# Performance work log

Measured on AMD Instinct MI355X. Metric: run time of the kernel, lower is better.

The kernel has to match this reference:

```python
import jax, jax.numpy as jnp
import numpy as np

HIDDEN = 128
N_HID = 7            # hidden_layers - 1 internal GELU blocks
N_TERMS = 2          # number of separable terms per side
N_IN = 1             # vars per term
B = 16384
STEP_SIZE = 0.1
NUM_STEPS = 1

# Forest-Ruth 4th-order symplectic coefficients
_K = 2.0 ** (1.0 / 3.0)
_C = (1.0 / (2.0 * (2.0 - _K)), (1.0 - _K) / (2.0 * (2.0 - _K)),
      (1.0 - _K) / (2.0 * (2.0 - _K)), 1.0 / (2.0 * (2.0 - _K)))
_D = (1.0 / (2.0 - _K), -_K / (2.0 - _K), 1.0 / (2.0 - _K), 0.0)


def _mlp(W0, b0, Wh, bh, Wo, bo, x):
    # x: [B, n_in] -> [B, 1]; torch GELU default is exact (erf)
    h = jax.nn.gelu(x @ W0 + b0, approximate=False)
    for i in range(N_HID):
        h = jax.nn.gelu(h @ Wh[i] + bh[i], approximate=False)
    return h @ Wo + bo


def _side_scalar(W0, b0, Wh, bh, Wo, bo, idx, x):
    # gather per-term feature subsets, run all term-MLPs batched via vmap,
    # sum over terms and batch (GradientWrapper takes grad of the summed scalar)
    xs = jnp.moveaxis(x[:, idx], 1, 0)            # [n_terms, B, n_in]
    outs = jax.vmap(_mlp)(W0, b0, Wh, bh, Wo, bo, xs)  # [n_terms, B, 1]
    return outs.sum()


def setup_inputs() -> dict:
    key = jax.random.key(0)
    ks = jax.random.split(key, 3)
    s = 0.05

    def pset(k):
        kk = jax.random.split(k, 6)
        return (
            jax.random.normal(kk[0], (N_TERMS, N_IN, HIDDEN), jnp.float32) * s,
            jax.random.normal(kk[1], (N_TERMS, HIDDEN), jnp.float32) * s,
            jax.random.normal(kk[2], (N_TERMS, N_HID, HIDDEN, HIDDEN), jnp.float32) * s,
            jax.random.normal(kk[3], (N_TERMS, N_HID, HIDDEN), jnp.float32) * s,
            jax.random.normal(kk[4], (N_TERMS, HIDDEN, 1), jnp.float32) * s,
            jax.random.normal(kk[5], (N_TERMS, 1), jnp.float32) * s,
        )

    lW0, lb0, lWh, lbh, lWo, lbo = pset(ks[0])
    rW0, rb0, rWh, rbh, rWo, rbo = pset(ks[1])
    X = jax.random.normal(ks[2], (B, 4), jnp.float32)
    left_idx = jnp.arange(N_TERMS, dtype=jnp.int32).reshape(N_TERMS, N_IN)
    right_idx = jnp.arange(N_TERMS, dtype=jnp.int32).reshape(N_TERMS, N_IN)
    return dict(X=X, lW0=lW0, lb0=lb0, lWh=lWh, lbh=lbh, lWo=lWo, lbo=lbo,
                rW0=rW0, rb0=rb0, rWh=rWh, rbh=rbh, rWo=rWo, rbo=rbo,
                left_idx=left_idx, right_idx=right_idx)


def reference(X, lW0, lb0, lWh, lbh, lWo, lbo,
              rW0, rb0, rWh, rbh, rWo, rbo, left_idx, right_idx):
    # H(q, p) = V(q) + T(p); left side = V(q), right side = T(p)
    dVdq = jax.grad(lambda q: _side_scalar(lW0, lb0, lWh, lbh, lWo, lbo, left_idx, q))
    dTdp = jax.grad(lambda p: _side_scalar(rW0, rb0, rWh, rbh, rWo, rbo, right_idx, p))
    dt = jnp.float32(STEP_SIZE)
    nq = X.shape[1] // 2
    q = X[:, :nq]
    p = X[:, nq:]
    for _ in range(NUM_STEPS):
        for c, d in zip(_C, _D):
            q = q + jnp.float32(c) * dt * dTdp(p)   # dq/dt =  dH/dp
            p = p - jnp.float32(d) * dt * dVdq(q)   # dp/dt = -dH/dq
    return jnp.concatenate((q, p), axis=1)
```

## Files before the change

kernel.cpp:

```cpp
#include <hip/hip_runtime.h>

#define NLAYER 7
#define IMGB 16384
#define WSCALE 16.0f

typedef __attribute__((ext_vector_type(2))) float float2v;
typedef __attribute__((ext_vector_type(4))) float float4v;
typedef __attribute__((ext_vector_type(4))) unsigned int uint4v;
typedef __attribute__((ext_vector_type(4))) int int4v;
typedef __attribute__((ext_vector_type(8))) int int8v;
typedef unsigned long long u64;

__device__ __forceinline__ float2v pk_fma(float2v a, float2v b, float2v c){
  return __builtin_elementwise_fma(a, b, c);
}
__device__ __forceinline__ float2v lo2(float4v v){ return (float2v){v[0], v[1]}; }
__device__ __forceinline__ float2v hi2(float4v v){ return (float2v){v[2], v[3]}; }

__device__ __forceinline__ unsigned pk4fp8(float v0, float v1, float v2, float v3){
  int w = __builtin_amdgcn_cvt_pk_fp8_f32(v0, v1, 0, false);
  w = __builtin_amdgcn_cvt_pk_fp8_f32(v2, v3, w, true);
  return (unsigned)w;
}
template<bool HI>
__device__ __forceinline__ float2v up2(unsigned w){
  return __builtin_amdgcn_cvt_pk_f32_fp8((int)w, HI);
}
__device__ __forceinline__ float4v mfma128(int8v a, int8v b){
  return __builtin_amdgcn_mfma_scale_f32_16x16x128_f8f6f4(
      a, b, (float4v){0.f,0.f,0.f,0.f}, 0, 0, 0, 0x7F7F7F7F, 0, 0x7F7F7F7F);
}
__device__ __forceinline__ void act2(float2v z, float2v& P16, float2v& gp16){
  const float2v c1v  = {6.3830764862829235f, 6.3830764862829235f};
  const float2v c3v  = {-1.0638460810704874f, -1.0638460810704874f};
  const float2v c33v = {-3.1915382432114624f, -3.1915382432114624f};
  const float2v v8   = {8.f, 8.f};
  float2v z2 = z * z;
  float2v u  = pk_fma(z2, c3v, c1v);
  P16 = pk_fma(z, u, v8);
  float2v Pd = pk_fma(z2, c33v, c1v);
  gp16 = pk_fma(z, Pd, P16);
}

__device__ __forceinline__ void gl2lds16(const unsigned char* g, unsigned char* l){
  __builtin_amdgcn_global_load_lds((const __attribute__((address_space(1))) unsigned int*)g,
                                   (__attribute__((address_space(3))) unsigned int*)l,
                                   16, 0, 0);
}

__device__ __forceinline__ int8v ld_op16(const unsigned char* lp, const unsigned char* hp){
  int4v lo = *(const int4v*)lp;
  int4v hi = *(const int4v*)hp;
  return __builtin_shufflevector(lo, hi, 0, 1, 2, 3, 4, 5, 6, 7);
}

__global__ __launch_bounds__(256)
void prep_weights(const float* __restrict__ lWh,
                  const float* __restrict__ rWh,
                  unsigned char* __restrict__ wbf)
{
  __shared__ __align__(16) unsigned char T[IMGB];
  const int b = blockIdx.x;
  const int net = b / NLAYER, L = b % NLAYER;
  const int side = net >> 1, term = net & 1;
  const float* src = (side ? rWh : lWh) + (size_t)((term*NLAYER + L)*128)*128;
  const int t = threadIdx.x;
  {
    const int k = t >> 1, n0 = (t & 1)*64;
    const float* row = src + k*128 + n0;
    #pragma unroll
    for (int c4 = 0; c4 < 4; ++c4){
      float4v f0 = *(const float4v*)(row + c4*16);
      float4v f1 = *(const float4v*)(row + c4*16 + 4);
      float4v f2 = *(const float4v*)(row + c4*16 + 8);
      float4v f3 = *(const float4v*)(row + c4*16 + 12);
      uint4v wv = { pk4fp8(f0[0]*WSCALE, f0[1]*WSCALE, f0[2]*WSCALE, f0[3]*WSCALE),
                    pk4fp8(f1[0]*WSCALE, f1[1]*WSCALE, f1[2]*WSCALE, f1[3]*WSCALE),
                    pk4fp8(f2[0]*WSCALE, f2[1]*WSCALE, f2[2]*WSCALE, f2[3]*WSCALE),
                    pk4fp8(f3[0]*WSCALE, f3[1]*WSCALE, f3[2]*WSCALE, f3[3]*WSCALE) };
      *(uint4v*)&T[k*128 + n0 + c4*16] = wv;
    }
  }
  __syncthreads();
  {
    const int n = t >> 1, c0 = (t & 1)*8;
    const int sw7 = n & 7;
    unsigned char* dst = wbf + ((size_t)b << 14) + n*128;
    #pragma unroll
    for (int c = 0; c < 8; ++c){
      const int c64 = c0 + c;
      const int kc = c64*8;
      u64 v = 0;
      #pragma unroll
      for (int j = 0; j < 8; ++j)
        v |= (u64)T[(kc + j)*128 + n] << (8*j);
      *(u64*)(dst + (((c64 >> 1) ^ sw7)*16) + (c64 & 1)*8) = v;
    }
  }
}

__global__ __launch_bounds__(256)
__attribute__((amdgpu_waves_per_eu(4, 4)))
void sympl_main(const float* __restrict__ X,
                const float* __restrict__ lW0, const float* __restrict__ lb0,
                const float* __restrict__ lbh, const float* __restrict__ lWo,
                const float* __restrict__ rW0, const float* __restrict__ rb0,
                const float* __restrict__ rbh, const float* __restrict__ rWo,
                const int* __restrict__ lidx, const int* __restrict__ ridx,
                const unsigned char* __restrict__ wbf,
                float* __restrict__ out)
{
  __shared__ __align__(16) unsigned char sW[2][IMGB];
  __shared__ __align__(16) unsigned char sH[8192];

  const int tid  = threadIdx.x;
  const int lane = tid & 63;
  const int w    = tid >> 6;
  const int m0   = lane & 15;
  const int q    = lane >> 4;
  const int g    = w & 1;
  const int ih   = w >> 1;
  const int col  = blockIdx.y;
  const int e0   = blockIdx.x * 32;
  const int r    = tid >> 3;
  const int sg   = tid & 7;
  const int r7   = r & 7;
  const int m06  = m0 & 6;
  const int m07  = m0 & 7;

  const int lt = (lidx[0] == col) ? 0 : 1;
  const int rt = (ridx[0] == col) ? 0 : 1;

  float qv = X[(e0 + r)*4 + col];
  float pv = X[(e0 + r)*4 + 2 + col];

  const float dt = 0.1f;
  const float C0 = 0.6756035959798289f, C1 = -0.17560359597982883f;
  const float D0 = 1.3512071919596578f, D1 = -1.7024143839193153f;
  const float is = 1.0f / 262144.0f;
  const float coefs[7] = { C0*dt*is, -D0*dt*is, C1*dt*is, -D1*dt*is,
                           C1*dt*is, -D0*dt*is, C0*dt*is };

  const float2v inv256v = {1.f/256.f, 1.f/256.f};
  const float2v inv64v  = {1.f/64.f, 1.f/64.f};

  const int lo16 = (m0 & 1) * 16;
  const int opo  = ((2*q) ^ m06) * 16;
  const unsigned char* pB0lo = sH + (g*16 + m0)*128 + opo + lo16;
  const unsigned char* pB0hi = sH + (g*16 + m0)*128 + opo + 16 - lo16;
  const unsigned char* pA0lo = sW[0] + (ih*64 + m0)*128 + opo + lo16;
  const unsigned char* pA0hi = sW[0] + (ih*64 + m0)*128 + opo + 16 - lo16;
  unsigned char* pHe = sH + (g*16 + m0)*128;
  unsigned char* pL0 = sH + r*128 + ((sg ^ r7)*16);
  const unsigned char* pRd = sH + 4096 + r*128 + ((sg ^ r7)*16);
  const int q4 = q * 4;
  const int eo0 = ((ih*4 + 0) ^ m07)*16 + q4;
  const int eo1 = ((ih*4 + 1) ^ m07)*16 + q4;
  const int eo2 = ((ih*4 + 2) ^ m07)*16 + q4;
  const int eo3 = ((ih*4 + 3) ^ m07)*16 + q4;

  {
    const unsigned char* src = wbf + (size_t)(2 + rt)*NLAYER*IMGB;
    #pragma unroll
    for (int it = 0; it < 4; ++it){
      int o = (it*256 + tid) * 16;
      gl2lds16(src + o, sW[0] + o);
    }
  }
  __syncthreads();

  int cur = 0;

  for (int ev = 0; ev < 7; ++ev){
    const bool isT = !(ev & 1);
    const int  term = isT ? rt : lt;
    const float* W0p = (isT ? rW0 : lW0) + term*128;
    const float* b0p = (isT ? rb0 : lb0) + term*128;
    const float* bhp = (isT ? rbh : lbh) + term*NLAYER*128;
    const float* Wop = (isT ? rWo : lWo) + term*128;
    const unsigned char* wimg = wbf + (size_t)(((isT ? 2 : 0) + term)*NLAYER)*IMGB;
    const int tnx = (ev & 1) ? rt : lt;
    const unsigned char* wimg_nx = wbf + (size_t)((((ev & 1) ? 2 : 0) + tnx)*NLAYER)*IMGB;

    {
      const float x = isT ? pv : qv;
      const float2v xv = {x, x};
      unsigned hw[4], dw[4];
      #pragma unroll
      for (int c = 0; c < 2; ++c){
        int n0 = sg*16 + c*8;
        float4v wa = *(const float4v*)(W0p + n0);
        float4v wb = *(const float4v*)(W0p + n0 + 4);
        float4v ba = *(const float4v*)(b0p + n0);
        float4v bb2 = *(const float4v*)(b0p + n0 + 4);
        float2v zp[4] = { pk_fma(xv, lo2(wa), lo2(ba)), pk_fma(xv, hi2(wa), hi2(ba)),
                          pk_fma(xv, lo2(wb), lo2(bb2)), pk_fma(xv, hi2(wb), hi2(bb2)) };
        float2v wp[4] = { lo2(wa), hi2(wa), lo2(wb), hi2(wb) };
        float Sh[8], Sd[8];
        #pragma unroll
        for (int pp = 0; pp < 4; ++pp){
          float2v P16, gp16; act2(zp[pp], P16, gp16);
          float2v h = zp[pp] * P16;
          float2v d = gp16 * wp[pp];
          Sh[pp*2] = h[0]; Sh[pp*2+1] = h[1];
          Sd[pp*2] = d[0]; Sd[pp*2+1] = d[1];
        }
        hw[c*2]   = pk4fp8(Sh[0],Sh[1],Sh[2],Sh[3]);
        hw[c*2+1] = pk4fp8(Sh[4],Sh[5],Sh[6],Sh[7]);
        dw[c*2]   = pk4fp8(Sd[0],Sd[1],Sd[2],Sd[3]);
        dw[c*2+1] = pk4fp8(Sd[4],Sd[5],Sd[6],Sd[7]);
      }
      *(uint4v*)(pL0)        = (uint4v){hw[0], hw[1], hw[2], hw[3]};
      *(uint4v*)(pL0 + 4096) = (uint4v){dw[0], dw[1], dw[2], dw[3]};
    }
    __syncthreads();

    for (int L = 0; L < NLAYER; ++L){
      const float* bias = bhp + L*128 + ih*64 + q4;
      float4v bv0 = *(const float4v*)(bias);
      float4v bv1 = *(const float4v*)(bias + 16);
      float4v bv2 = *(const float4v*)(bias + 32);
      float4v bv3 = *(const float4v*)(bias + 48);

      if (!(ev == 6 && L == 6)){
        const unsigned char* nsrc = (L < 6) ? (wimg + (size_t)(L+1)*IMGB) : wimg_nx;
        unsigned char* dW = sW[cur^1];
        #pragma unroll
        for (int it = 0; it < 4; ++it){
          int o = (it*256 + tid) * 16;
          gl2lds16(nsrc + o, dW + o);
        }
      }

      const int bufo = cur ? IMGB : 0;
      const unsigned char* pAcLo = pA0lo + bufo;
      const unsigned char* pAcHi = pA0hi + bufo;
      int8v b0 = ld_op16(pB0lo, pB0hi);
      int8v b1 = ld_op16(pB0lo + 4096, pB0hi + 4096);
      float4v acc[4][2];
      #pragma unroll
      for (int i = 0; i < 4; ++i){
        int8v a = ld_op16(pAcLo + i*2048, pAcHi + i*2048);
        acc[i][0] = mfma128(a, b0);
        acc[i][1] = mfma128(a, b1);
      }

      asm volatile("s_waitcnt lgkmcnt(0)" ::: "memory");
      __builtin_amdgcn_s_barrier();
      asm volatile("" ::: "memory");

      const bool last = (L == NLAYER-1);
      #define EPI(i, bvv, eo) { \
        float2v za = pk_fma(lo2(acc[i][0]), inv256v, lo2(bvv)); \
        float2v zb = pk_fma(hi2(acc[i][0]), inv256v, hi2(bvv)); \
        float2v ta = lo2(acc[i][1]) * inv64v; \
        float2v tb = hi2(acc[i][1]) * inv64v; \
        float2v Pa, ga, Pb, gb; \
        act2(za, Pa, ga); \
        act2(zb, Pb, gb); \
        float2v ha = za * Pa, hb = zb * Pb; \
        float2v da = ga * ta, db = gb * tb; \
        if (!last) *(unsigned*)(pHe + eo) = pk4fp8(ha[0], ha[1], hb[0], hb[1]); \
        *(unsigned*)(pHe + 4096 + eo) = pk4fp8(da[0], da[1], db[0], db[1]); \
      }
      EPI(0, bv0, eo0)
      EPI(1, bv1, eo1)
      EPI(2, bv2, eo2)
      EPI(3, bv3, eo3)
      #undef EPI

      __syncthreads();
      cur ^= 1;
    }

    {
      uint4v dvv = *(const uint4v*)(pRd);
      float2v sv = {0.f, 0.f};
      float4v woa = *(const float4v*)(Wop + sg*16);
      float4v wob = *(const float4v*)(Wop + sg*16 + 4);
      float4v woc = *(const float4v*)(Wop + sg*16 + 8);
      float4v wod = *(const float4v*)(Wop + sg*16 + 12);
      sv = pk_fma(up2<false>(dvv[0]), lo2(woa), sv);
      sv = pk_fma(up2<true>(dvv[0]),  hi2(woa), sv);
      sv = pk_fma(up2<false>(dvv[1]), lo2(wob), sv);
      sv = pk_fma(up2<true>(dvv[1]),  hi2(wob), sv);
      sv = pk_fma(up2<false>(dvv[2]), lo2(woc), sv);
      sv = pk_fma(up2<true>(dvv[2]),  hi2(woc), sv);
      sv = pk_fma(up2<false>(dvv[3]), lo2(wod), sv);
      sv = pk_fma(up2<true>(dvv[3]),  hi2(wod), sv);
      float s = sv[0] + sv[1];
      s += __shfl_xor(s, 1);
      s += __shfl_xor(s, 2);
      s += __shfl_xor(s, 4);
      if (isT) qv += coefs[ev] * s;
      else     pv += coefs[ev] * s;
    }
    __syncthreads();
  }

  if (sg == 0){
    out[(e0 + r)*4 + col]     = qv;
    out[(e0 + r)*4 + 2 + col] = pv;
  }
}

extern "C" void kernel_launch(void* const* d_in, const int* in_sizes, int n_in,
                              void* d_out, int out_size, void* d_ws, size_t ws_size,
                              hipStream_t stream)
{
  const float* X   = (const float*)d_in[0];
  const float* lW0 = (const float*)d_in[1];
  const float* lb0 = (const float*)d_in[2];
  const float* lWh = (const float*)d_in[3];
  const float* lbh = (const float*)d_in[4];
  const float* lWo = (const float*)d_in[5];
  const float* rW0 = (const float*)d_in[7];
  const float* rb0 = (const float*)d_in[8];
  const float* rWh = (const float*)d_in[9];
  const float* rbh = (const float*)d_in[10];
  const float* rWo = (const float*)d_in[11];
  const int*   li  = (const int*)d_in[13];
  const int*   ri  = (const int*)d_in[14];
  unsigned char* wbf = (unsigned char*)d_ws;
  float* out = (float*)d_out;
  const int B = in_sizes[0] / 4;

  hipLaunchKernelGGL(prep_weights, dim3(4*NLAYER), dim3(256), 0, stream,
                     lWh, rWh, wbf);
  hipLaunchKernelGGL(sympl_main, dim3(B/32, 2), dim3(256), 0, stream,
                     X, lW0, lb0, lbh, lWo, rW0, rb0, rbh, rWo, li, ri, wbf, out);
}
```

Baseline: 192.2 us.

## Load weight operands directly into registers and double-buffer activations in LDS

The prep kernel now writes weights in a per-lane MFMA operand order, so each lane fetches its A fragments straight from global memory into registers. This replaces the global-to-LDS weight staging and its double buffer. The hidden-activation LDS buffer is double-buffered by layer parity, which drops one barrier per layer and the barrier after each evaluation. LDS use shrinks, which may help occupancy, but the next layer's weights now come from global/L2 into VGPRs and their latency may be exposed before the next layer's MFMAs.

```diff
diff --git a/kernel.cpp b/kernel.cpp
--- a/kernel.cpp
+++ b/kernel.cpp
@@ -40,12 +40,6 @@
   P16 = pk_fma(z, u, v8);
   float2v Pd = pk_fma(z2, c33v, c1v);
   gp16 = pk_fma(z, Pd, P16);
-}
-
-__device__ __forceinline__ void gl2lds16(const unsigned char* g, unsigned char* l){
-  __builtin_amdgcn_global_load_lds((const __attribute__((address_space(1))) unsigned int*)g,
-                                   (__attribute__((address_space(3))) unsigned int*)l,
-                                   16, 0, 0);
 }
 
 __device__ __forceinline__ int8v ld_op16(const unsigned char* lp, const unsigned char* hp){
@@ -84,8 +78,8 @@
   __syncthreads();
   {
     const int n = t >> 1, c0 = (t & 1)*8;
-    const int sw7 = n & 7;
-    unsigned char* dst = wbf + ((size_t)b << 14) + n*128;
+    const int ihn = n >> 6, in_ = (n >> 4) & 3, m0n = n & 15;
+    unsigned char* dst = wbf + ((size_t)b << 14);
     #pragma unroll
     for (int c = 0; c < 8; ++c){
       const int c64 = c0 + c;
@@ -94,7 +88,8 @@
       #pragma unroll
       for (int j = 0; j < 8; ++j)
         v |= (u64)T[(kc + j)*128 + n] << (8*j);
-      *(u64*)(dst + (((c64 >> 1) ^ sw7)*16) + (c64 & 1)*8) = v;
+      const int off = ((ihn*4 + (c64 >> 2))*16 + m0n)*128 + in_*32 + (kc & 31);
+      *(u64*)(dst + off) = v;
     }
   }
 }
@@ -110,8 +105,7 @@
                 const unsigned char* __restrict__ wbf,
                 float* __restrict__ out)
 {
-  __shared__ __align__(16) unsigned char sW[2][IMGB];
-  __shared__ __align__(16) unsigned char sH[8192];
+  __shared__ __align__(16) unsigned char sH[2*8192];
 
   const int tid  = threadIdx.x;
   const int lane = tid & 63;
@@ -148,28 +142,23 @@
   const int opo  = ((2*q) ^ m06) * 16;
   const unsigned char* pB0lo = sH + (g*16 + m0)*128 + opo + lo16;
   const unsigned char* pB0hi = sH + (g*16 + m0)*128 + opo + 16 - lo16;
-  const unsigned char* pA0lo = sW[0] + (ih*64 + m0)*128 + opo + lo16;
-  const unsigned char* pA0hi = sW[0] + (ih*64 + m0)*128 + opo + 16 - lo16;
   unsigned char* pHe = sH + (g*16 + m0)*128;
   unsigned char* pL0 = sH + r*128 + ((sg ^ r7)*16);
-  const unsigned char* pRd = sH + 4096 + r*128 + ((sg ^ r7)*16);
+  const unsigned char* pRd = sH + 8192 + 4096 + r*128 + ((sg ^ r7)*16);
   const int q4 = q * 4;
-  const int eo0 = ((ih*4 + 0) ^ m07)*16 + q4;
-  const int eo1 = ((ih*4 + 1) ^ m07)*16 + q4;
-  const int eo2 = ((ih*4 + 2) ^ m07)*16 + q4;
-  const int eo3 = ((ih*4 + 3) ^ m07)*16 + q4;
-
+  unsigned char* pE0 = pHe + ((ih*4 + 0) ^ m07)*16 + q4;
+  unsigned char* pE1 = pHe + ((ih*4 + 1) ^ m07)*16 + q4;
+  unsigned char* pE2 = pHe + ((ih*4 + 2) ^ m07)*16 + q4;
+  unsigned char* pE3 = pHe + ((ih*4 + 3) ^ m07)*16 + q4;
+
+  const int laneAoff = ((ih*4 + q)*16 + m0)*128;
+
+  int4v aC[8];
   {
-    const unsigned char* src = wbf + (size_t)(2 + rt)*NLAYER*IMGB;
+    const unsigned char* asrc = wbf + (size_t)(2 + rt)*NLAYER*IMGB + laneAoff;
     #pragma unroll
-    for (int it = 0; it < 4; ++it){
-      int o = (it*256 + tid) * 16;
-      gl2lds16(src + o, sW[0] + o);
-    }
-  }
-  __syncthreads();
-
-  int cur = 0;
+    for (int i = 0; i < 8; ++i) aC[i] = *(const int4v*)(asrc + i*16);
+  }
 
   for (int ev = 0; ev < 7; ++ev){
     const bool isT = !(ev & 1);
@@ -213,44 +202,39 @@
       *(uint4v*)(pL0)        = (uint4v){hw[0], hw[1], hw[2], hw[3]};
       *(uint4v*)(pL0 + 4096) = (uint4v){dw[0], dw[1], dw[2], dw[3]};
     }
-    __syncthreads();
-
+    asm volatile("s_waitcnt lgkmcnt(0)" ::: "memory");
+    __builtin_amdgcn_s_barrier();
+    asm volatile("" ::: "memory");
+
+    #pragma unroll
     for (int L = 0; L < NLAYER; ++L){
+      const int rdo = (L & 1) * 8192;
+      const int wro = rdo ^ 8192;
+
       const float* bias = bhp + L*128 + ih*64 + q4;
       float4v bv0 = *(const float4v*)(bias);
       float4v bv1 = *(const float4v*)(bias + 16);
       float4v bv2 = *(const float4v*)(bias + 32);
       float4v bv3 = *(const float4v*)(bias + 48);
 
-      if (!(ev == 6 && L == 6)){
-        const unsigned char* nsrc = (L < 6) ? (wimg + (size_t)(L+1)*IMGB) : wimg_nx;
-        unsigned char* dW = sW[cur^1];
-        #pragma unroll
-        for (int it = 0; it < 4; ++it){
-          int o = (it*256 + tid) * 16;
-          gl2lds16(nsrc + o, dW + o);
-        }
-      }
-
-      const int bufo = cur ? IMGB : 0;
-      const unsigned char* pAcLo = pA0lo + bufo;
-      const unsigned char* pAcHi = pA0hi + bufo;
-      int8v b0 = ld_op16(pB0lo, pB0hi);
-      int8v b1 = ld_op16(pB0lo + 4096, pB0hi + 4096);
+      int8v b0 = ld_op16(pB0lo + rdo, pB0hi + rdo);
+      int8v b1 = ld_op16(pB0lo + rdo + 4096, pB0hi + rdo + 4096);
       float4v acc[4][2];
       #pragma unroll
       for (int i = 0; i < 4; ++i){
-        int8v a = ld_op16(pAcLo + i*2048, pAcHi + i*2048);
+        int8v a = __builtin_shufflevector(aC[2*i], aC[2*i+1], 0, 1, 2, 3, 4, 5, 6, 7);
         acc[i][0] = mfma128(a, b0);
         acc[i][1] = mfma128(a, b1);
       }
 
-      asm volatile("s_waitcnt lgkmcnt(0)" ::: "memory");
-      __builtin_amdgcn_s_barrier();
-      asm volatile("" ::: "memory");
+      if (!(ev == 6 && L == 6)){
+        const unsigned char* nsrc = ((L < 6) ? (wimg + (size_t)(L+1)*IMGB) : wimg_nx) + laneAoff;
+        #pragma unroll
+        for (int i = 0; i < 8; ++i) aC[i] = *(const int4v*)(nsrc + i*16);
+      }
 
       const bool last = (L == NLAYER-1);
-      #define EPI(i, bvv, eo) { \
+      #define EPI(i, bvv, pe) { \
         float2v za = pk_fma(lo2(acc[i][0]), inv256v, lo2(bvv)); \
         float2v zb = pk_fma(hi2(acc[i][0]), inv256v, hi2(bvv)); \
         float2v ta = lo2(acc[i][1]) * inv64v; \
@@ -260,17 +244,18 @@
         act2(zb, Pb, gb); \
         float2v ha = za * Pa, hb = zb * Pb; \
         float2v da = ga * ta, db = gb * tb; \
-        if (!last) *(unsigned*)(pHe + eo) = pk4fp8(ha[0], ha[1], hb[0], hb[1]); \
-        *(unsigned*)(pHe + 4096 + eo) = pk4fp8(da[0], da[1], db[0], db[1]); \
+        if (!last) *(unsigned*)(pe + wro) = pk4fp8(ha[0], ha[1], hb[0], hb[1]); \
+        *(unsigned*)(pe + wro + 4096) = pk4fp8(da[0], da[1], db[0], db[1]); \
       }
-      EPI(0, bv0, eo0)
-      EPI(1, bv1, eo1)
-      EPI(2, bv2, eo2)
-      EPI(3, bv3, eo3)
+      EPI(0, bv0, pE0)
+      EPI(1, bv1, pE1)
+      EPI(2, bv2, pE2)
+      EPI(3, bv3, pE3)
       #undef EPI
 
-      __syncthreads();
-      cur ^= 1;
+      asm volatile("s_waitcnt lgkmcnt(0)" ::: "memory");
+      __builtin_amdgcn_s_barrier();
+      asm volatile("" ::: "memory");
     }
 
     {
@@ -295,7 +280,6 @@
       if (isT) qv += coefs[ev] * s;
       else     pv += coefs[ev] * s;
     }
-    __syncthreads();
   }
 
   if (sg == 0){
```

Result: slower. 309.6 us (+61.0%).
